# Optimization experiments

Hardware: AMD Instinct MI355X
Metric: run time of the kernel (lower is better)

## Reference

```python
import jax, jax.numpy as jnp
import numpy as np

N = 50000      # nodes
E = 800000     # edges
IN_C = 128
HID = 96
OUT_C = 40
L = 8          # num_layers
ALPHA = 0.1
THETA = 0.5
DROPOUT = 0.5


def setup_inputs() -> dict:
    key = jax.random.key(0)
    ks = jax.random.split(key, 6)
    x = jax.random.normal(ks[0], (N, IN_C), dtype=jnp.float32)
    edge_index = jax.random.randint(ks[1], (2, E), 0, N, dtype=jnp.int64)
    proj_w = jax.random.normal(ks[2], (IN_C, HID), dtype=jnp.float32) / np.sqrt(IN_C)
    proj_b = jnp.zeros((HID,), dtype=jnp.float32)
    conv_ws = jax.random.normal(ks[3], (L, HID, HID), dtype=jnp.float32) / np.sqrt(HID)
    out_w = jax.random.normal(ks[4], (2 * HID, OUT_C), dtype=jnp.float32) / np.sqrt(2 * HID)
    out_b = jnp.zeros((OUT_C,), dtype=jnp.float32)
    return {"x": x, "edge_index": edge_index, "proj_w": proj_w, "proj_b": proj_b,
            "conv_ws": conv_ws, "out_w": out_w, "out_b": out_b}


def reference(x, edge_index, proj_w, proj_b, conv_ws, out_w, out_b):
    # --- GCN normalization with self loops (computed once, as GCN2Conv caches it) ---
    loops = jnp.arange(N, dtype=edge_index.dtype)
    src = jnp.concatenate([edge_index[0], loops])   # [E+N]
    dst = jnp.concatenate([edge_index[1], loops])
    deg = jax.ops.segment_sum(jnp.ones(E + N, dtype=x.dtype), dst, num_segments=N)
    dis = jax.lax.rsqrt(deg)                        # deg >= 1 due to self loops
    norm = dis[src] * dis[dst]                      # [E+N]

    h0 = x @ proj_w + proj_b                        # [N, HID]
    h = h0
    key = jax.random.key(42)
    for k in range(L):
        delta = 1.0 / 2 ** k
        kq, ke, kd, key = jax.random.split(key, 4)
        # dithered quantization
        b = (jax.random.uniform(kq, h.shape, dtype=h.dtype) - 0.5) * delta
        h_q = jnp.floor((h + b) / delta) * delta - b
        # GCN2Conv: propagate + initial residual + identity mapping (shared weights)
        agg = jax.ops.segment_sum(h_q[src] * norm[:, None], dst, num_segments=N)
        t = (1.0 - ALPHA) * agg + ALPHA * h0
        beta = float(np.log(THETA / (k + 1) + 1.0))
        h = (1.0 - beta) * t + beta * (t @ conv_ws[k])
        # gaussian noise + relu
        h = jax.nn.relu(h + 0.01 * jax.random.normal(ke, h.shape, dtype=h.dtype))
        if k != L - 1:
            keep = 1.0 - DROPOUT
            mask = jax.random.bernoulli(kd, keep, h.shape)
            h = jnp.where(mask, h / keep, 0.0)
    return jnp.concatenate([h0, h], axis=-1) @ out_w + out_b
```

## Files before the change

### kernel.cpp

```cpp
#include <hip/hip_runtime.h>
#include <hip/hip_fp16.h>
#include <cstdint>
#include <cmath>

#define HID 96
#define INC 128
#define OUTC 40

__device__ __forceinline__ unsigned rotl32d(unsigned x, int r){ return (x<<r)|(x>>(32-r)); }

__device__ __forceinline__ void tf2x32_dev(unsigned k0, unsigned k1, unsigned x0, unsigned x1,
                                           unsigned &y0, unsigned &y1){
  unsigned ks2 = k0 ^ k1 ^ 0x1BD11BDAu;
  x0 += k0; x1 += k1;
#define TFR(r) { x0 += x1; x1 = rotl32d(x1, r); x1 ^= x0; }
  TFR(13) TFR(15) TFR(26) TFR(6)   x0 += k1;  x1 += ks2 + 1u;
  TFR(17) TFR(29) TFR(16) TFR(24)  x0 += ks2; x1 += k0 + 2u;
  TFR(13) TFR(15) TFR(26) TFR(6)   x0 += k0;  x1 += k1 + 3u;
  TFR(17) TFR(29) TFR(16) TFR(24)  x0 += k1;  x1 += ks2 + 4u;
  TFR(13) TFR(15) TFR(26) TFR(6)   x0 += ks2; x1 += k0 + 5u;
#undef TFR
  y0 = x0; y1 = x1;
}

__device__ __forceinline__ unsigned tf_bits(unsigned k0, unsigned k1, unsigned idx){
  unsigned y0, y1; tf2x32_dev(k0, k1, 0u, idx, y0, y1); return y0 ^ y1;
}

__device__ __forceinline__ float u01_from_bits(unsigned bits){
  return __uint_as_float((bits >> 9) | 0x3f800000u) - 1.0f;
}

__device__ __forceinline__ float erfinv_xla(float x){
  float w = -log1pf(-x*x);
  float p;
  if (w < 5.0f){
    w = w - 2.5f;
    p = 2.81022636e-08f;
    p = fmaf(p,w, 3.43273939e-07f);
    p = fmaf(p,w,-3.5233877e-06f);
    p = fmaf(p,w,-4.39150654e-06f);
    p = fmaf(p,w, 0.00021858087f);
    p = fmaf(p,w,-0.00125372503f);
    p = fmaf(p,w,-0.00417768164f);
    p = fmaf(p,w, 0.246640727f);
    p = fmaf(p,w, 1.50140941f);
  } else {
    w = sqrtf(w) - 3.0f;
    p = -0.000200214257f;
    p = fmaf(p,w, 0.000100950558f);
    p = fmaf(p,w, 0.00134934322f);
    p = fmaf(p,w,-0.00367342844f);
    p = fmaf(p,w, 0.00573950773f);
    p = fmaf(p,w,-0.0076224613f);
    p = fmaf(p,w, 0.00943887047f);
    p = fmaf(p,w, 1.00167406f);
    p = fmaf(p,w, 2.83297682f);
  }
  return p*x;
}

__global__ void k_detect(const unsigned* __restrict__ raw, int* flag){
  unsigned v = raw[2*threadIdx.x + 1];
  unsigned long long m = __ballot(v == 0u);
  if (threadIdx.x == 0) *flag = (m == 0xFFFFFFFFFFFFFFFFull) ? 1 : 0;
}

__global__ void k_convcount(const unsigned* __restrict__ raw, const int* __restrict__ flag,
                            int E, int* __restrict__ src, int* __restrict__ dst,
                            int* __restrict__ cnt){
  int e = blockIdx.x*256 + threadIdx.x; if (e >= E) return;
  int s, d;
  if (*flag){ s = (int)raw[2*(size_t)e]; d = (int)raw[2*((size_t)E + e)]; }
  else      { const int* r = (const int*)raw; s = r[e]; d = r[E + e]; }
  src[e] = s; dst[e] = d;
  atomicAdd(&cnt[d], 1);
}

__global__ void k_psum_histo(const int* __restrict__ cnt, int N,
                             int* __restrict__ psum, int* __restrict__ bcnt){
  __shared__ int sh[256];
  __shared__ int lh[64];
  int tid = threadIdx.x; int n = blockIdx.x*256 + tid;
  int v = (n < N) ? cnt[n] : 0;
  sh[tid] = v;
  if (tid < 64) lh[tid] = 0;
  __syncthreads();
  if (n < N) atomicAdd(&lh[min(v, 63)], 1);
  for (int off = 128; off > 0; off >>= 1){
    __syncthreads();
    if (tid < off) sh[tid] += sh[tid + off];
  }
  __syncthreads();
  if (tid == 0) psum[blockIdx.x] = sh[0];
  if (tid < 64){
    int c = lh[tid];
    if (c > 0) atomicAdd(&bcnt[tid], c);
  }
}

__global__ void k_scan2(int* __restrict__ psum, int nb, int* __restrict__ bcnt){
  __shared__ int sh[256];
  __shared__ int sb[64];
  int tid = threadIdx.x;
  int v = (tid < nb) ? psum[tid] : 0;
  sh[tid] = v;
  if (tid < 64) sb[tid] = bcnt[tid];
  __syncthreads();
  for (int off = 1; off < 256; off <<= 1){
    int t = (tid >= off) ? sh[tid - off] : 0;
    __syncthreads();
    sh[tid] += t;
    __syncthreads();
  }
  if (tid < nb) psum[tid] = sh[tid] - v;
  if (tid < 64){
    int off = 0;
    for (int b2 = tid+1; b2 < 64; b2++) off += sb[b2];
    bcnt[tid] = off;
  }
}

__global__ void k_rowptr_perm(const int* __restrict__ cnt, const int* __restrict__ psum,
                              int N, int E, int* __restrict__ rowptr, float* __restrict__ dis,
                              int* __restrict__ bcnt, int* __restrict__ perm){
  __shared__ int sh[256];
  __shared__ int lh[64];
  int tid = threadIdx.x; int n = blockIdx.x*256 + tid;
  int v = (n < N) ? cnt[n] : 0;
  sh[tid] = v;
  if (tid < 64) lh[tid] = 0;
  __syncthreads();
  int b = min(v, 63), r = 0;
  if (n < N) r = atomicAdd(&lh[b], 1);
  for (int off = 1; off < 256; off <<= 1){
    int t = (tid >= off) ? sh[tid - off] : 0;
    __syncthreads();
    sh[tid] += t;
    __syncthreads();
  }
  if (n < N){
    rowptr[n] = psum[blockIdx.x] + sh[tid] - v;
    dis[n] = 1.0f / sqrtf((float)(v + 1));
  }
  if (n == N-1) rowptr[N] = E;
  if (tid < 64){
    int c = lh[tid];
    lh[tid] = (c > 0) ? atomicAdd(&bcnt[tid], c) : 0;
  }
  __syncthreads();
  if (n < N) perm[lh[b] + r] = n;
}

__global__ void k_fill(const int* __restrict__ src, const int* __restrict__ dst, int E,
                       const int* __restrict__ rowptr, int* __restrict__ cnt,
                       const float* __restrict__ dis,
                       int* __restrict__ csr_src, float* __restrict__ csr_w){
  int e = blockIdx.x*256 + threadIdx.x; if (e >= E) return;
  int d = dst[e], s = src[e];
  int pos = atomicAdd(&cnt[d], 1);
  int slot = rowptr[d] + pos;
  csr_src[slot] = s;
  csr_w[slot] = dis[s]*dis[d];
}

__global__ __launch_bounds__(256) void k_h0(
  const float* __restrict__ x, const float* __restrict__ W, const float* __restrict__ bias,
  float* __restrict__ h0, __half* __restrict__ hq, unsigned kq0, unsigned kq1, int N)
{
  __shared__ float xs[64*65];
  __shared__ float wsh[64*96];
  int tid = threadIdx.x; int n0 = blockIdx.x*64;
  int cg = tid & 15, ng = tid >> 4; int c0 = cg*6;
  float acc[4][6];
#pragma unroll
  for (int i=0;i<4;i++) for (int j=0;j<6;j++) acc[i][j]=0.f;
  for (int kc=0; kc<2; kc++){
    if (kc) __syncthreads();
    for (int q=tid; q<1536; q+=256)
      ((float4*)wsh)[q] = ((const float4*)(W + kc*64*96))[q];
    for (int q=tid; q<1024; q+=256){
      int g=q*4; int r=g>>6, col=g&63;
      int n=n0+r; int ns = n<N ? n : N-1;
      float4 v = ((const float4*)(x + (size_t)ns*128 + kc*64))[col>>2];
      xs[r*65+col]=v.x; xs[r*65+col+1]=v.y; xs[r*65+col+2]=v.z; xs[r*65+col+3]=v.w;
    }
    __syncthreads();
    for (int k=0;k<64;k++){
      float wv[6];
#pragma unroll
      for (int j=0;j<6;j++) wv[j]=wsh[k*96 + c0 + j];
#pragma unroll
      for (int i=0;i<4;i++){
        float xv = xs[(ng*4+i)*65 + k];
#pragma unroll
        for (int j=0;j<6;j++) acc[i][j] = fmaf(xv, wv[j], acc[i][j]);
      }
    }
  }
#pragma unroll
  for (int i=0;i<4;i++){
    int n = n0 + ng*4 + i; if (n >= N) continue;
#pragma unroll
    for (int j=0;j<6;j++){
      int c = c0 + j; int p = n*96 + c;
      float v = acc[i][j] + bias[c];
      h0[p] = v;
      unsigned bq = tf_bits(kq0, kq1, (unsigned)p);
      float b = u01_from_bits(bq) - 0.5f;
      hq[(size_t)n*96 + c] = __float2half_rn(floorf(v + b) - b);
    }
  }
}

__global__ __launch_bounds__(256, 4) void k_layer(
  const __half* __restrict__ hq_in, const float* __restrict__ h0, const float* __restrict__ dis,
  const int* __restrict__ rowptr, const int* __restrict__ csr_src, const float* __restrict__ csr_w,
  const int* __restrict__ perm, const float* __restrict__ W,
  float betaf, float ombf,
  unsigned ke0, unsigned ke1, unsigned kd0, unsigned kd1,
  unsigned kq0, unsigned kq1, float delta_n, float invdelta_n,
  int do_dropout, int write_h,
  __half* __restrict__ hq_out, float* __restrict__ h_out, int N)
{
  __shared__ float ts[64*100];
  __shared__ float wsh[24*96];
  __shared__ int rowmap[64];
  int tid = threadIdx.x;
  int tx = tid & 31, ty = tid >> 5;
  int n0 = blockIdx.x*64;

  const uint2* hq2 = (const uint2*)hq_in;
  const float4* h04 = (const float4*)h0;

#pragma unroll 1
  for (int pass = 0; pass < 8; pass++){
    int r = pass*8 + ty;
    int row = n0 + r;
    int n = (row < N) ? perm[row] : -1;
    if (tx == 0) rowmap[r] = n;
    if (tx < 24){
      float4 o = make_float4(0.f, 0.f, 0.f, 0.f);
      if (n >= 0){
        float d = dis[n];
        int lo = rowptr[n], hi = rowptr[n+1];
        uint2 sraw = hq2[(size_t)n*24 + tx];
        float2 s01 = __half22float2(*(__half2*)&sraw.x);
        float2 s23 = __half22float2(*(__half2*)&sraw.y);
        float dd = d*d;
        float ax = s01.x*dd, ay = s01.y*dd, az = s23.x*dd, aw = s23.y*dd;
        for (int s = lo; s < hi; s += 8){
          int   sn[8];
          float w[8];
#pragma unroll
          for (int j = 0; j < 8; j++){
            bool hv = (s + j) < hi;
            sn[j] = hv ? csr_src[s + j] : csr_src[s];
            w[j]  = hv ? csr_w[s + j]   : 0.0f;
          }
          uint2 g[8];
#pragma unroll
          for (int j = 0; j < 8; j++) g[j] = hq2[(size_t)sn[j]*24 + tx];
#pragma unroll
          for (int j = 0; j < 8; j++){
            float2 f01 = __half22float2(*(__half2*)&g[j].x);
            float2 f23 = __half22float2(*(__half2*)&g[j].y);
            ax = fmaf(f01.x, w[j], ax); ay = fmaf(f01.y, w[j], ay);
            az = fmaf(f23.x, w[j], az); aw = fmaf(f23.y, w[j], aw);
          }
        }
        float4 hz = h04[(size_t)n*24 + tx];
        o.x = 0.9f*ax + 0.1f*hz.x;
        o.y = 0.9f*ay + 0.1f*hz.y;
        o.z = 0.9f*az + 0.1f*hz.z;
        o.w = 0.9f*aw + 0.1f*hz.w;
      }
      *((float4*)&ts[r*100 + tx*4]) = o;
    }
  }

  int cg = tid & 7, ng = tid >> 3;
  int c0 = cg * 12;
  int r0 = ng * 2;
  float acc[2][12];
#pragma unroll
  for (int i = 0; i < 2; i++)
#pragma unroll
    for (int j = 0; j < 12; j++) acc[i][j] = 0.f;

  for (int chunk = 0; chunk < 4; chunk++){
    __syncthreads();
    for (int q = tid; q < 576; q += 256)
      ((float4*)wsh)[q] = ((const float4*)(W + chunk*24*96))[q];
    __syncthreads();
#pragma unroll 4
    for (int kk = 0; kk < 24; kk++){
      int k = chunk*24 + kk;
      float4 w0 = *((const float4*)&wsh[kk*96 + c0]);
      float4 w1 = *((const float4*)&wsh[kk*96 + c0 + 4]);
      float4 w2 = *((const float4*)&wsh[kk*96 + c0 + 8]);
      float xv0 = ts[r0*100 + k];
      float xv1 = ts[(r0+1)*100 + k];
      acc[0][0] = fmaf(xv0, w0.x, acc[0][0]);  acc[0][1] = fmaf(xv0, w0.y, acc[0][1]);
      acc[0][2] = fmaf(xv0, w0.z, acc[0][2]);  acc[0][3] = fmaf(xv0, w0.w, acc[0][3]);
      acc[0][4] = fmaf(xv0, w1.x, acc[0][4]);  acc[0][5] = fmaf(xv0, w1.y, acc[0][5]);
      acc[0][6] = fmaf(xv0, w1.z, acc[0][6]);  acc[0][7] = fmaf(xv0, w1.w, acc[0][7]);
      acc[0][8] = fmaf(xv0, w2.x, acc[0][8]);  acc[0][9] = fmaf(xv0, w2.y, acc[0][9]);
      acc[0][10]= fmaf(xv0, w2.z, acc[0][10]); acc[0][11]= fmaf(xv0, w2.w, acc[0][11]);
      acc[1][0] = fmaf(xv1, w0.x, acc[1][0]);  acc[1][1] = fmaf(xv1, w0.y, acc[1][1]);
      acc[1][2] = fmaf(xv1, w0.z, acc[1][2]);  acc[1][3] = fmaf(xv1, w0.w, acc[1][3]);
      acc[1][4] = fmaf(xv1, w1.x, acc[1][4]);  acc[1][5] = fmaf(xv1, w1.y, acc[1][5]);
      acc[1][6] = fmaf(xv1, w1.z, acc[1][6]);  acc[1][7] = fmaf(xv1, w1.w, acc[1][7]);
      acc[1][8] = fmaf(xv1, w2.x, acc[1][8]);  acc[1][9] = fmaf(xv1, w2.y, acc[1][9]);
      acc[1][10]= fmaf(xv1, w2.z, acc[1][10]); acc[1][11]= fmaf(xv1, w2.w, acc[1][11]);
    }
  }

  const float LO = __uint_as_float(0xBF7FFFFFu);
#pragma unroll
  for (int i = 0; i < 2; i++){
    int n = rowmap[r0 + i]; if (n < 0) continue;
    float res[12];
#pragma unroll
    for (int j = 0; j < 12; j++){
      int c = c0 + j; int p = n*96 + c;
      float tv = ts[(r0+i)*100 + c];
      float hv = ombf*tv + betaf*acc[i][j];
      unsigned be = tf_bits(ke0, ke1, (unsigned)p);
      float uv = fmaxf(LO, u01_from_bits(be)*2.0f + LO);
      hv += 0.01f * (1.41421356f * erfinv_xla(uv));
      hv = fmaxf(hv, 0.0f);
      if (do_dropout){
        unsigned bd = tf_bits(kd0, kd1, (unsigned)p);
        hv = (bd < 0x80000000u) ? hv*2.0f : 0.0f;
      }
      if (!write_h){
        unsigned bq = tf_bits(kq0, kq1, (unsigned)p);
        float b = (u01_from_bits(bq) - 0.5f)*delta_n;
        hv = floorf((hv + b)*invdelta_n)*delta_n - b;
      }
      res[j] = hv;
    }
    if (write_h){
      float* dst = h_out + (size_t)n*96 + c0;
#pragma unroll
      for (int j4 = 0; j4 < 3; j4++)
        *((float4*)&dst[j4*4]) = make_float4(res[j4*4], res[j4*4+1], res[j4*4+2], res[j4*4+3]);
    } else {
      uint2* dst = (uint2*)(hq_out + (size_t)n*96 + c0);
#pragma unroll
      for (int j4 = 0; j4 < 3; j4++){
        unsigned lo2 = (unsigned)__half_as_ushort(__float2half_rn(res[j4*4+0]))
                     | ((unsigned)__half_as_ushort(__float2half_rn(res[j4*4+1])) << 16);
        unsigned hi2 = (unsigned)__half_as_ushort(__float2half_rn(res[j4*4+2]))
                     | ((unsigned)__half_as_ushort(__float2half_rn(res[j4*4+3])) << 16);
        dst[j4] = make_uint2(lo2, hi2);
      }
    }
  }
}

__global__ __launch_bounds__(256) void k_final(
  const float* __restrict__ h0, const float* __restrict__ h,
  const float* __restrict__ W, const float* __restrict__ bias,
  float* __restrict__ out, int N)
{
  __shared__ float xs[64*97];
  __shared__ float wsh[96*40];
  int tid = threadIdx.x; int n0 = blockIdx.x*64;
  int cg = tid & 7, ng = tid >> 3; int c0 = cg*5;
  float acc[2][5];
#pragma unroll
  for (int i=0;i<2;i++) for (int j=0;j<5;j++) acc[i][j]=0.f;
  for (int ph=0; ph<2; ph++){
    if (ph) __syncthreads();
    const float* xsrc = ph ? h : h0;
    for (int q=tid; q<960; q+=256)
      ((float4*)wsh)[q] = ((const float4*)(W + ph*96*40))[q];
    for (int q=tid; q<1536; q+=256){
      int g=q*4; int r=g/96, col=g%96;
      int n=n0+r; int ns = n<N ? n : N-1;
      float4 v = ((const float4*)(xsrc + (size_t)ns*96))[col>>2];
      xs[r*97+col]=v.x; xs[r*97+col+1]=v.y; xs[r*97+col+2]=v.z; xs[r*97+col+3]=v.w;
    }
    __syncthreads();
    for (int k=0;k<96;k++){
      float wv[5];
#pragma unroll
      for (int j=0;j<5;j++) wv[j]=wsh[k*40 + c0 + j];
#pragma unroll
      for (int i=0;i<2;i++){
        float xv = xs[(ng*2+i)*97 + k];
#pragma unroll
        for (int j=0;j<5;j++) acc[i][j] = fmaf(xv, wv[j], acc[i][j]);
      }
    }
  }
#pragma unroll
  for (int i=0;i<2;i++){
    int n = n0 + ng*2 + i; if (n >= N) continue;
#pragma unroll
    for (int j=0;j<5;j++)
      out[(size_t)n*40 + c0 + j] = acc[i][j] + bias[c0 + j];
  }
}

static void tf_host(uint32_t k0, uint32_t k1, uint32_t x0, uint32_t x1,
                    uint32_t &y0, uint32_t &y1){
  uint32_t ks2 = k0 ^ k1 ^ 0x1BD11BDAu;
  x0 += k0; x1 += k1;
  auto R = [&](int r){ x0 += x1; x1 = (x1<<r)|(x1>>(32-r)); x1 ^= x0; };
  R(13);R(15);R(26);R(6);   x0 += k1;  x1 += ks2 + 1u;
  R(17);R(29);R(16);R(24);  x0 += ks2; x1 += k0 + 2u;
  R(13);R(15);R(26);R(6);   x0 += k0;  x1 += k1 + 3u;
  R(17);R(29);R(16);R(24);  x0 += k1;  x1 += ks2 + 4u;
  R(13);R(15);R(26);R(6);   x0 += ks2; x1 += k0 + 5u;
  y0 = x0; y1 = x1;
}

extern "C" void kernel_launch(void* const* d_in, const int* in_sizes, int n_in,
                              void* d_out, int out_size, void* d_ws, size_t ws_size,
                              hipStream_t stream)
{
  const float*    x       = (const float*)d_in[0];
  const unsigned* eraw    = (const unsigned*)d_in[1];
  const float*    proj_w  = (const float*)d_in[2];
  const float*    proj_b  = (const float*)d_in[3];
  const float*    conv_w  = (const float*)d_in[4];
  const float*    out_w   = (const float*)d_in[5];
  const float*    out_b   = (const float*)d_in[6];
  float* out = (float*)d_out;

  const int N = in_sizes[0] / INC;
  const int E = in_sizes[1] / 2;
  const size_t NH = (size_t)N * HID;

  float*  ws     = (float*)d_ws;
  float*  h0     = ws;
  __half* hqA    = (__half*)(h0 + NH);
  __half* hqB    = hqA + NH;
  float*  hb     = (float*)(hqB + NH);
  float*  dis    = hb + NH;
  int*    cnt    = (int*)(dis + N);
  int*    rowptr = cnt + N;
  int*    csr_src= rowptr + (N + 1);
  float*  csr_w  = (float*)(csr_src + E);
  int*    srcb   = (int*)(csr_w + E);
  int*    dstb   = srcb + E;
  int*    flag   = dstb + E;
  int*    perm   = flag + 1;
  int*    bcnt   = perm + N;
  int*    psum   = bcnt + 64;
  (void)ws_size; (void)n_in; (void)out_size;

  uint32_t kq[8][2], ke[8][2], kd[8][2];
  {
    uint32_t K0 = 0u, K1 = 42u;
    for (int k = 0; k < 8; k++){
      uint32_t y0, y1;
      tf_host(K0, K1, 0u, 0u, y0, y1); kq[k][0]=y0; kq[k][1]=y1;
      tf_host(K0, K1, 0u, 1u, y0, y1); ke[k][0]=y0; ke[k][1]=y1;
      tf_host(K0, K1, 0u, 2u, y0, y1); kd[k][0]=y0; kd[k][1]=y1;
      tf_host(K0, K1, 0u, 3u, y0, y1); K0=y0; K1=y1;
    }
  }

  const int gE  = (E + 255)/256;
  const int gN  = (N + 255)/256;
  const int gMM = (N + 63)/64;

  hipMemsetAsync(cnt, 0, (size_t)N*4, stream);
  hipMemsetAsync(bcnt, 0, 64*4, stream);
  k_detect <<<1, 64, 0, stream>>>(eraw, flag);
  k_convcount<<<gE, 256, 0, stream>>>(eraw, flag, E, srcb, dstb, cnt);
  k_psum_histo<<<gN, 256, 0, stream>>>(cnt, N, psum, bcnt);
  k_scan2  <<<1, 256, 0, stream>>>(psum, gN, bcnt);
  k_rowptr_perm<<<gN, 256, 0, stream>>>(cnt, psum, N, E, rowptr, dis, bcnt, perm);
  hipMemsetAsync(cnt, 0, (size_t)N*4, stream);
  k_fill   <<<gE, 256, 0, stream>>>(srcb, dstb, E, rowptr, cnt, dis, csr_src, csr_w);

  k_h0<<<gMM, 256, 0, stream>>>(x, proj_w, proj_b, h0, hqA, kq[0][0], kq[0][1], N);

  for (int k = 0; k < 8; k++){
    double bd = log(0.5/(double)(k+1) + 1.0);
    float betaf = (float)bd;
    float ombf  = (float)(1.0 - bd);
    int last = (k == 7);
    float dn  = 1.0f/(float)(1 << (k+1));
    float idn = (float)(1 << (k+1));
    const __half* hin  = (k & 1) ? hqB : hqA;
    __half*       hout = (k & 1) ? hqA : hqB;
    k_layer<<<gMM, 256, 0, stream>>>(hin, h0, dis, rowptr, csr_src, csr_w, perm,
      conv_w + (size_t)k*HID*HID, betaf, ombf,
      ke[k][0], ke[k][1], kd[k][0], kd[k][1],
      last?0u:kq[k+1][0], last?0u:kq[k+1][1], dn, idn,
      !last, last, hout, hb, N);
  }

  k_final<<<gMM, 256, 0, stream>>>(h0, hb, out_w, out_b, out, N);
}
```

Measured before the change: 1.001 ms.

## Interleave CSR edges, store h0 in fp16, shrink weight tile for occupancy

Packs each edge's source index and normalization weight into one 8-byte record, so the gather loop issues one load per edge instead of two. Stores the initial projection h0 in half precision, halving its read traffic in every layer and in the final projection. Halves the shared weight chunk and raises the launch-bounds occupancy hint from 4 to 5 blocks. The fp16 h0 adds rounding error to the residual and output terms, and the smaller weight tiles double the number of block syncs in the layer GEMM.

```diff
diff --git a/kernel.cpp b/kernel.cpp
--- a/kernel.cpp
+++ b/kernel.cpp
@@ -155,18 +155,16 @@
 __global__ void k_fill(const int* __restrict__ src, const int* __restrict__ dst, int E,
                        const int* __restrict__ rowptr, int* __restrict__ cnt,
                        const float* __restrict__ dis,
-                       int* __restrict__ csr_src, float* __restrict__ csr_w){
+                       uint2* __restrict__ edges){
   int e = blockIdx.x*256 + threadIdx.x; if (e >= E) return;
   int d = dst[e], s = src[e];
   int pos = atomicAdd(&cnt[d], 1);
-  int slot = rowptr[d] + pos;
-  csr_src[slot] = s;
-  csr_w[slot] = dis[s]*dis[d];
+  edges[rowptr[d] + pos] = make_uint2((unsigned)s, __float_as_uint(dis[s]*dis[d]));
 }
 
 __global__ __launch_bounds__(256) void k_h0(
   const float* __restrict__ x, const float* __restrict__ W, const float* __restrict__ bias,
-  float* __restrict__ h0, __half* __restrict__ hq, unsigned kq0, unsigned kq1, int N)
+  __half* __restrict__ h0h, __half* __restrict__ hq, unsigned kq0, unsigned kq1, int N)
 {
   __shared__ float xs[64*65];
   __shared__ float wsh[64*96];
@@ -205,7 +203,7 @@
     for (int j=0;j<6;j++){
       int c = c0 + j; int p = n*96 + c;
       float v = acc[i][j] + bias[c];
-      h0[p] = v;
+      h0h[(size_t)n*96 + c] = __float2half_rn(v);
       unsigned bq = tf_bits(kq0, kq1, (unsigned)p);
       float b = u01_from_bits(bq) - 0.5f;
       hq[(size_t)n*96 + c] = __float2half_rn(floorf(v + b) - b);
@@ -213,9 +211,9 @@
   }
 }
 
-__global__ __launch_bounds__(256, 4) void k_layer(
-  const __half* __restrict__ hq_in, const float* __restrict__ h0, const float* __restrict__ dis,
-  const int* __restrict__ rowptr, const int* __restrict__ csr_src, const float* __restrict__ csr_w,
+__global__ __launch_bounds__(256, 5) void k_layer(
+  const __half* __restrict__ hq_in, const __half* __restrict__ h0h, const float* __restrict__ dis,
+  const int* __restrict__ rowptr, const uint2* __restrict__ edges,
   const int* __restrict__ perm, const float* __restrict__ W,
   float betaf, float ombf,
   unsigned ke0, unsigned ke1, unsigned kd0, unsigned kd1,
@@ -224,14 +222,14 @@
   __half* __restrict__ hq_out, float* __restrict__ h_out, int N)
 {
   __shared__ float ts[64*100];
-  __shared__ float wsh[24*96];
+  __shared__ float wsh[12*96];
   __shared__ int rowmap[64];
   int tid = threadIdx.x;
   int tx = tid & 31, ty = tid >> 5;
   int n0 = blockIdx.x*64;
 
   const uint2* hq2 = (const uint2*)hq_in;
-  const float4* h04 = (const float4*)h0;
+  const uint2* h02 = (const uint2*)h0h;
 
 #pragma unroll 1
   for (int pass = 0; pass < 8; pass++){
@@ -250,30 +248,32 @@
         float dd = d*d;
         float ax = s01.x*dd, ay = s01.y*dd, az = s23.x*dd, aw = s23.y*dd;
         for (int s = lo; s < hi; s += 8){
-          int   sn[8];
-          float w[8];
+          uint2 ew[8];
 #pragma unroll
           for (int j = 0; j < 8; j++){
             bool hv = (s + j) < hi;
-            sn[j] = hv ? csr_src[s + j] : csr_src[s];
-            w[j]  = hv ? csr_w[s + j]   : 0.0f;
+            ew[j] = edges[hv ? (s + j) : s];
+            if (!hv) ew[j].y = 0u;
           }
           uint2 g[8];
 #pragma unroll
-          for (int j = 0; j < 8; j++) g[j] = hq2[(size_t)sn[j]*24 + tx];
+          for (int j = 0; j < 8; j++) g[j] = hq2[(size_t)ew[j].x*24 + tx];
 #pragma unroll
           for (int j = 0; j < 8; j++){
+            float w = __uint_as_float(ew[j].y);
             float2 f01 = __half22float2(*(__half2*)&g[j].x);
             float2 f23 = __half22float2(*(__half2*)&g[j].y);
-            ax = fmaf(f01.x, w[j], ax); ay = fmaf(f01.y, w[j], ay);
-            az = fmaf(f23.x, w[j], az); aw = fmaf(f23.y, w[j], aw);
+            ax = fmaf(f01.x, w, ax); ay = fmaf(f01.y, w, ay);
+            az = fmaf(f23.x, w, az); aw = fmaf(f23.y, w, aw);
           }
         }
-        float4 hz = h04[(size_t)n*24 + tx];
-        o.x = 0.9f*ax + 0.1f*hz.x;
-        o.y = 0.9f*ay + 0.1f*hz.y;
-        o.z = 0.9f*az + 0.1f*hz.z;
-        o.w = 0.9f*aw + 0.1f*hz.w;
+        uint2 hraw = h02[(size_t)n*24 + tx];
+        float2 h01 = __half22float2(*(__half2*)&hraw.x);
+        float2 h23 = __half22float2(*(__half2*)&hraw.y);
+        o.x = 0.9f*ax + 0.1f*h01.x;
+        o.y = 0.9f*ay + 0.1f*h01.y;
+        o.z = 0.9f*az + 0.1f*h23.x;
+        o.w = 0.9f*aw + 0.1f*h23.y;
       }
       *((float4*)&ts[r*100 + tx*4]) = o;
     }
@@ -288,14 +288,14 @@
 #pragma unroll
     for (int j = 0; j < 12; j++) acc[i][j] = 0.f;
 
-  for (int chunk = 0; chunk < 4; chunk++){
-    __syncthreads();
-    for (int q = tid; q < 576; q += 256)
-      ((float4*)wsh)[q] = ((const float4*)(W + chunk*24*96))[q];
+  for (int chunk = 0; chunk < 8; chunk++){
+    __syncthreads();
+    for (int q = tid; q < 288; q += 256)
+      ((float4*)wsh)[q] = ((const float4*)(W + chunk*12*96))[q];
     __syncthreads();
 #pragma unroll 4
-    for (int kk = 0; kk < 24; kk++){
-      int k = chunk*24 + kk;
+    for (int kk = 0; kk < 12; kk++){
+      int k = chunk*12 + kk;
       float4 w0 = *((const float4*)&wsh[kk*96 + c0]);
       float4 w1 = *((const float4*)&wsh[kk*96 + c0 + 4]);
       float4 w2 = *((const float4*)&wsh[kk*96 + c0 + 8]);
@@ -361,7 +361,7 @@
 }
 
 __global__ __launch_bounds__(256) void k_final(
-  const float* __restrict__ h0, const float* __restrict__ h,
+  const __half* __restrict__ h0h, const float* __restrict__ h,
   const float* __restrict__ W, const float* __restrict__ bias,
   float* __restrict__ out, int N)
 {
@@ -374,13 +374,20 @@
   for (int i=0;i<2;i++) for (int j=0;j<5;j++) acc[i][j]=0.f;
   for (int ph=0; ph<2; ph++){
     if (ph) __syncthreads();
-    const float* xsrc = ph ? h : h0;
     for (int q=tid; q<960; q+=256)
       ((float4*)wsh)[q] = ((const float4*)(W + ph*96*40))[q];
     for (int q=tid; q<1536; q+=256){
       int g=q*4; int r=g/96, col=g%96;
       int n=n0+r; int ns = n<N ? n : N-1;
-      float4 v = ((const float4*)(xsrc + (size_t)ns*96))[col>>2];
+      float4 v;
+      if (ph){
+        v = ((const float4*)(h + (size_t)ns*96))[col>>2];
+      } else {
+        uint2 raw = ((const uint2*)h0h)[(size_t)ns*24 + (col>>2)];
+        float2 a = __half22float2(*(__half2*)&raw.x);
+        float2 b = __half22float2(*(__half2*)&raw.y);
+        v = make_float4(a.x, a.y, b.x, b.y);
+      }
       xs[r*97+col]=v.x; xs[r*97+col+1]=v.y; xs[r*97+col+2]=v.z; xs[r*97+col+3]=v.w;
     }
     __syncthreads();
@@ -435,22 +442,21 @@
   const int E = in_sizes[1] / 2;
   const size_t NH = (size_t)N * HID;
 
-  float*  ws     = (float*)d_ws;
-  float*  h0     = ws;
-  __half* hqA    = (__half*)(h0 + NH);
-  __half* hqB    = hqA + NH;
-  float*  hb     = (float*)(hqB + NH);
-  float*  dis    = hb + NH;
-  int*    cnt    = (int*)(dis + N);
-  int*    rowptr = cnt + N;
-  int*    csr_src= rowptr + (N + 1);
-  float*  csr_w  = (float*)(csr_src + E);
-  int*    srcb   = (int*)(csr_w + E);
-  int*    dstb   = srcb + E;
-  int*    flag   = dstb + E;
-  int*    perm   = flag + 1;
-  int*    bcnt   = perm + N;
-  int*    psum   = bcnt + 64;
+  char* wp = (char*)d_ws;
+  __half* h0h   = (__half*)wp;            wp += NH*2;
+  __half* hqA   = (__half*)wp;            wp += NH*2;
+  __half* hqB   = (__half*)wp;            wp += NH*2;
+  float*  hb    = (float*)wp;             wp += NH*4;
+  float*  dis   = (float*)wp;             wp += (size_t)N*4;
+  int*    cnt   = (int*)wp;               wp += (size_t)N*4;
+  int*    rowptr= (int*)wp;               wp += (size_t)(N+4)*4;
+  uint2*  edges = (uint2*)wp;             wp += (size_t)E*8;
+  int*    srcb  = (int*)wp;               wp += (size_t)E*4;
+  int*    dstb  = (int*)wp;               wp += (size_t)E*4;
+  int*    flag  = (int*)wp;               wp += 16;
+  int*    perm  = (int*)wp;               wp += (size_t)N*4;
+  int*    bcnt  = (int*)wp;               wp += 64*4;
+  int*    psum  = (int*)wp;               wp += 256*4;
   (void)ws_size; (void)n_in; (void)out_size;
 
   uint32_t kq[8][2], ke[8][2], kd[8][2];
@@ -477,9 +483,9 @@
   k_scan2  <<<1, 256, 0, stream>>>(psum, gN, bcnt);
   k_rowptr_perm<<<gN, 256, 0, stream>>>(cnt, psum, N, E, rowptr, dis, bcnt, perm);
   hipMemsetAsync(cnt, 0, (size_t)N*4, stream);
-  k_fill   <<<gE, 256, 0, stream>>>(srcb, dstb, E, rowptr, cnt, dis, csr_src, csr_w);
-
-  k_h0<<<gMM, 256, 0, stream>>>(x, proj_w, proj_b, h0, hqA, kq[0][0], kq[0][1], N);
+  k_fill   <<<gE, 256, 0, stream>>>(srcb, dstb, E, rowptr, cnt, dis, edges);
+
+  k_h0<<<gMM, 256, 0, stream>>>(x, proj_w, proj_b, h0h, hqA, kq[0][0], kq[0][1], N);
 
   for (int k = 0; k < 8; k++){
     double bd = log(0.5/(double)(k+1) + 1.0);
@@ -490,12 +496,12 @@
     float idn = (float)(1 << (k+1));
     const __half* hin  = (k & 1) ? hqB : hqA;
     __half*       hout = (k & 1) ? hqA : hqB;
-    k_layer<<<gMM, 256, 0, stream>>>(hin, h0, dis, rowptr, csr_src, csr_w, perm,
+    k_layer<<<gMM, 256, 0, stream>>>(hin, h0h, dis, rowptr, edges, perm,
       conv_w + (size_t)k*HID*HID, betaf, ombf,
       ke[k][0], ke[k][1], kd[k][0], kd[k][1],
       last?0u:kq[k+1][0], last?0u:kq[k+1][1], dn, idn,
       !last, last, hout, hb, N);
   }
 
-  k_final<<<gMM, 256, 0, stream>>>(h0, hb, out_w, out_b, out, N);
-}
+  k_final<<<gMM, 256, 0, stream>>>(h0h, hb, out_w, out_b, out, N);
+}
```

New measurement: 1.071 ms. 6.9% more time.
